# Kernel tuning notes

Hardware: AMD Instinct MI355X
Metric: run time of the kernel (lower is better)

## Reference

```python
import jax, jax.numpy as jnp
import numpy as np

MASK_FILL = -1e10
LOG_2PI = float(np.log(2.0 * np.pi))


def setup_inputs() -> dict:
    key = jax.random.key(0)
    k1, k2, k3 = jax.random.split(key, 3)
    bs, seq_len, emb_dim = 32, 512, 512
    T = 2048
    emb = jax.random.normal(k1, (bs, seq_len, emb_dim), dtype=jnp.float32)
    # positive durations; rescale so the max total duration over the batch == T exactly,
    # matching torch's T = sum(durations).int().max()
    d = jax.random.uniform(k2, (bs, seq_len), dtype=jnp.float32, minval=0.5, maxval=1.0)
    d = d * (T / jnp.max(jnp.sum(d, axis=1)))
    log_sigma = jax.random.normal(k3, (1,), dtype=jnp.float32) * 0.1
    return {"emb": emb, "durations": d, "log_sigma": log_sigma, "T": T}


def reference(emb, durations, log_sigma, T):
    # emb: (bs, S, E); durations: (bs, S); log_sigma: (1,); T: static int
    bs, S, E = emb.shape
    ls = log_sigma[0]
    sigma = jnp.exp(ls)
    # Gaussian centers per token: cumsum - 0.5*dur  -> (bs, S)
    centers = jnp.cumsum(durations, axis=1) - 0.5 * durations
    t = jnp.arange(T, dtype=emb.dtype)  # frame indices (T,)
    # Normal(loc=centers, scale=sigma).log_prob(t + 0.5)  -> (bs, T, S)
    z = (t[None, :, None] + 0.5 - centers[:, None, :]) / sigma
    logp = -0.5 * z * z - ls - 0.5 * LOG_2PI
    # mask out zero-duration tokens
    logp = jnp.where((durations == 0.0)[:, None, :], MASK_FILL, logp)
    w = jax.nn.softmax(logp, axis=2)  # (bs, T, S)
    x = jnp.einsum('bts,bse->bte', w, emb)  # (bs, T, E)
    total = jnp.sum(durations, axis=1)  # (bs,)
    out_mask = t[None, :] < total[:, None]  # (bs, T) bool
    return x, out_mask
```

## Files before the change

### kernel.cpp

```cpp
#include <hip/hip_runtime.h>
#include <math.h>

#define BS 32
#define S_TOK 512
#define E_DIM 512
#define T_FR 2048
#define FPB 32
#define WMAX 36
#define THRESH -25.0f


typedef float vfloat4 __attribute__((ext_vector_type(4)));

struct RowMeta { float m; float inv_l; int lo; int cnt; };

__global__ __launch_bounds__(64) void scan_kernel(
    const float* __restrict__ dur,
    float* __restrict__ centers,
    float* __restrict__ totals) {
  int b = blockIdx.x;
  int lane = threadIdx.x;
  const float* d = dur + b * S_TOK;
  int base = lane * 8;
  double local[8];
  double run = 0.0;
#pragma unroll
  for (int i = 0; i < 8; ++i) { run += (double)d[base + i]; local[i] = run; }
  double sum = run;
#pragma unroll
  for (int off = 1; off < 64; off <<= 1) {
    double v = __shfl_up(sum, off, 64);
    if (lane >= off) sum += v;
  }
  double excl = sum - run;
#pragma unroll
  for (int i = 0; i < 8; ++i) {
    centers[b * S_TOK + base + i] =
        (float)(excl + local[i] - 0.5 * (double)d[base + i]);
  }
  if (lane == 63) totals[b] = (float)sum;
}

__global__ __launch_bounds__(256) void meta_kernel(
    const float* __restrict__ centers,
    const float* __restrict__ log_sigma,
    RowMeta* __restrict__ meta) {
  int b = blockIdx.x >> 3;
  int t = ((blockIdx.x & 7) << 8) + threadIdx.x;

  __shared__ float cbS[S_TOK];
  for (int i = threadIdx.x; i < S_TOK; i += 256)
    cbS[i] = centers[b * S_TOK + i];
  __syncthreads();

  float inv_sigma = expf(-log_sigma[0]);
  float tq = (float)t + 0.5f;

  auto V = [&](int s) {
    float z = (tq - cbS[s]) * inv_sigma;
    return -0.5f * z * z;
  };

  int lo = 0, hi = S_TOK;
  while (lo < hi) {
    int mid = (lo + hi) >> 1;
    if (cbS[mid] < tq) lo = mid + 1; else hi = mid;
  }
  int best; float m;
  if (lo == 0) { best = 0; m = V(0); }
  else if (lo == S_TOK) { best = S_TOK - 1; m = V(best); }
  else {
    float va = V(lo - 1), vb = V(lo);
    if (va >= vb) { best = lo - 1; m = va; } else { best = lo; m = vb; }
  }

  int wl = best, wh = best;
  while (wl > 0 && V(wl - 1) > m + THRESH) --wl;
  while (wh < S_TOK - 1 && V(wh + 1) > m + THRESH) ++wh;

  float l = 0.0f;
  for (int s = wl; s <= wh; ++s) l += expf(V(s) - m);

  RowMeta mt;
  mt.m = m;
  mt.inv_l = 1.0f / l;
  mt.lo = wl;
  mt.cnt = wh - wl + 1;
  meta[b * T_FR + t] = mt;
}

__global__ __launch_bounds__(256) void fused_kernel(
    const float* __restrict__ emb,
    const float* __restrict__ centers,
    const float* __restrict__ log_sigma,
    const RowMeta* __restrict__ meta,
    const float* __restrict__ totals,
    float* __restrict__ x,
    float* __restrict__ mask_out) {
  int id = blockIdx.x;
  int sw = ((id & 7) << 8) + (id >> 3);
  int b = sw >> 6;
  int t0 = (sw & 63) << 5;

  int tid = threadIdx.x;
  int half = tid >> 7;
  int lane = tid & 127;

  __shared__ float wT[WMAX][FPB];
  __shared__ RowMeta metaS[FPB];

  if (tid < FPB) metaS[tid] = meta[b * T_FR + t0 + tid];
  __syncthreads();

  int ulo = metaS[0].lo, uhi = metaS[0].lo + metaS[0].cnt - 1;
#pragma unroll
  for (int f = 1; f < FPB; ++f) {
    ulo = min(ulo, metaS[f].lo);
    uhi = max(uhi, metaS[f].lo + metaS[f].cnt - 1);
  }
  int cnt = min(uhi - ulo + 1, WMAX);

  float inv_sigma = expf(-log_sigma[0]);
  const float* cb = centers + b * S_TOK;

  for (int k = tid; k < cnt * FPB; k += 256) {
    int i = k >> 5, f = k & 31;
    float c = cb[ulo + i];
    float tqf = (float)(t0 + f) + 0.5f;
    float z = (tqf - c) * inv_sigma;
    float v = -0.5f * z * z;
    float e = expf(v - metaS[f].m) * metaS[f].inv_l;
    wT[i][f] = (v - metaS[f].m > THRESH) ? e : 0.0f;
  }
  __syncthreads();

  const vfloat4* e4 =
      (const vfloat4*)emb + ((size_t)(b * S_TOK + ulo)) * (E_DIM / 4) + lane;
  vfloat4 acc[16];
#pragma unroll
  for (int f = 0; f < 16; ++f) acc[f] = (vfloat4){0.f, 0.f, 0.f, 0.f};

  vfloat4 vcur = e4[0];
  vfloat4 vnext = e4[(size_t)min(1, cnt - 1) * (E_DIM / 4)];
  for (int i = 0; i < cnt; ++i) {
    vfloat4 vfut = e4[(size_t)min(i + 2, cnt - 1) * (E_DIM / 4)];
    const vfloat4* wp = (const vfloat4*)&wT[i][half << 4];
    vfloat4 w0 = wp[0], w1 = wp[1], w2 = wp[2], w3 = wp[3];
    acc[0] += w0.x * vcur;  acc[1] += w0.y * vcur;
    acc[2] += w0.z * vcur;  acc[3] += w0.w * vcur;
    acc[4] += w1.x * vcur;  acc[5] += w1.y * vcur;
    acc[6] += w1.z * vcur;  acc[7] += w1.w * vcur;
    acc[8] += w2.x * vcur;  acc[9] += w2.y * vcur;
    acc[10] += w2.z * vcur; acc[11] += w2.w * vcur;
    acc[12] += w3.x * vcur; acc[13] += w3.y * vcur;
    acc[14] += w3.z * vcur; acc[15] += w3.w * vcur;
    vcur = vnext; vnext = vfut;
  }

  vfloat4* xp = (vfloat4*)x +
      ((size_t)(b * T_FR + t0 + (half << 4))) * (E_DIM / 4) + lane;
#pragma unroll
  for (int f = 0; f < 16; ++f)
    xp[(size_t)f * (E_DIM / 4)] = acc[f];

  if (tid < FPB) {
    int t = t0 + tid;
    mask_out[b * T_FR + t] = ((float)t < totals[b]) ? 1.0f : 0.0f;
  }
}

extern "C" void kernel_launch(void* const* d_in, const int* in_sizes, int n_in,
                              void* d_out, int out_size, void* d_ws,
                              size_t ws_size, hipStream_t stream) {
  const float* emb = (const float*)d_in[0];
  const float* dur = (const float*)d_in[1];
  const float* log_sigma = (const float*)d_in[2];

  float* x = (float*)d_out;
  float* mask_out = x + (size_t)BS * T_FR * E_DIM;

  float* centers = (float*)d_ws;
  float* totals = centers + BS * S_TOK;
  RowMeta* meta = (RowMeta*)(totals + 64);

  scan_kernel<<<BS, 64, 0, stream>>>(dur, centers, totals);
  meta_kernel<<<BS * 8, 256, 0, stream>>>(centers, log_sigma, meta);
  fused_kernel<<<(BS * T_FR) / FPB, 256, 0, stream>>>(
      emb, centers, log_sigma, meta, totals, x, mask_out);
}
```

Before: 174.9 us.

## Fuse scan and meta kernels into the main weighted-sum kernel

New measurement: 169.7 us. -3.0%, faster.

```diff
diff --git a/kernel.cpp b/kernel.cpp
--- a/kernel.cpp
+++ b/kernel.cpp
@@ -10,91 +10,15 @@
 #define THRESH -25.0f
 
 
+
 typedef float vfloat4 __attribute__((ext_vector_type(4)));
 
 struct RowMeta { float m; float inv_l; int lo; int cnt; };
 
-__global__ __launch_bounds__(64) void scan_kernel(
+__global__ __launch_bounds__(256) void fused_all(
+    const float* __restrict__ emb,
     const float* __restrict__ dur,
-    float* __restrict__ centers,
-    float* __restrict__ totals) {
-  int b = blockIdx.x;
-  int lane = threadIdx.x;
-  const float* d = dur + b * S_TOK;
-  int base = lane * 8;
-  double local[8];
-  double run = 0.0;
-#pragma unroll
-  for (int i = 0; i < 8; ++i) { run += (double)d[base + i]; local[i] = run; }
-  double sum = run;
-#pragma unroll
-  for (int off = 1; off < 64; off <<= 1) {
-    double v = __shfl_up(sum, off, 64);
-    if (lane >= off) sum += v;
-  }
-  double excl = sum - run;
-#pragma unroll
-  for (int i = 0; i < 8; ++i) {
-    centers[b * S_TOK + base + i] =
-        (float)(excl + local[i] - 0.5 * (double)d[base + i]);
-  }
-  if (lane == 63) totals[b] = (float)sum;
-}
-
-__global__ __launch_bounds__(256) void meta_kernel(
-    const float* __restrict__ centers,
     const float* __restrict__ log_sigma,
-    RowMeta* __restrict__ meta) {
-  int b = blockIdx.x >> 3;
-  int t = ((blockIdx.x & 7) << 8) + threadIdx.x;
-
-  __shared__ float cbS[S_TOK];
-  for (int i = threadIdx.x; i < S_TOK; i += 256)
-    cbS[i] = centers[b * S_TOK + i];
-  __syncthreads();
-
-  float inv_sigma = expf(-log_sigma[0]);
-  float tq = (float)t + 0.5f;
-
-  auto V = [&](int s) {
-    float z = (tq - cbS[s]) * inv_sigma;
-    return -0.5f * z * z;
-  };
-
-  int lo = 0, hi = S_TOK;
-  while (lo < hi) {
-    int mid = (lo + hi) >> 1;
-    if (cbS[mid] < tq) lo = mid + 1; else hi = mid;
-  }
-  int best; float m;
-  if (lo == 0) { best = 0; m = V(0); }
-  else if (lo == S_TOK) { best = S_TOK - 1; m = V(best); }
-  else {
-    float va = V(lo - 1), vb = V(lo);
-    if (va >= vb) { best = lo - 1; m = va; } else { best = lo; m = vb; }
-  }
-
-  int wl = best, wh = best;
-  while (wl > 0 && V(wl - 1) > m + THRESH) --wl;
-  while (wh < S_TOK - 1 && V(wh + 1) > m + THRESH) ++wh;
-
-  float l = 0.0f;
-  for (int s = wl; s <= wh; ++s) l += expf(V(s) - m);
-
-  RowMeta mt;
-  mt.m = m;
-  mt.inv_l = 1.0f / l;
-  mt.lo = wl;
-  mt.cnt = wh - wl + 1;
-  meta[b * T_FR + t] = mt;
-}
-
-__global__ __launch_bounds__(256) void fused_kernel(
-    const float* __restrict__ emb,
-    const float* __restrict__ centers,
-    const float* __restrict__ log_sigma,
-    const RowMeta* __restrict__ meta,
-    const float* __restrict__ totals,
     float* __restrict__ x,
     float* __restrict__ mask_out) {
   int id = blockIdx.x;
@@ -106,10 +30,70 @@
   int half = tid >> 7;
   int lane = tid & 127;
 
+  __shared__ float cbS[S_TOK];
   __shared__ float wT[WMAX][FPB];
   __shared__ RowMeta metaS[FPB];
+  __shared__ double wsumS[4];
+  __shared__ float totalS;
 
-  if (tid < FPB) metaS[tid] = meta[b * T_FR + t0 + tid];
+  {
+    const float* dp = dur + b * S_TOK;
+    int i2 = tid << 1;
+    double d0 = (double)dp[i2];
+    double d1 = (double)dp[i2 + 1];
+    double pair = d0 + d1;
+    double run = pair;
+#pragma unroll
+    for (int off = 1; off < 64; off <<= 1) {
+      double v = __shfl_up(run, off, 64);
+      if ((tid & 63) >= off) run += v;
+    }
+    int w = tid >> 6;
+    if ((tid & 63) == 63) wsumS[w] = run;
+    __syncthreads();
+    double wexcl = 0.0;
+#pragma unroll
+    for (int k = 0; k < 3; ++k) wexcl += (k < w) ? wsumS[k] : 0.0;
+    double incl = wexcl + run;
+    double excl = incl - pair;
+    cbS[i2]     = (float)(excl + d0 - 0.5 * d0);
+    cbS[i2 + 1] = (float)(excl + (d0 + d1) - 0.5 * d1);
+    if (tid == 255) totalS = (float)incl;
+  }
+  __syncthreads();
+
+  float inv_sigma = expf(-log_sigma[0]);
+
+  if (tid < FPB) {
+    float tq = (float)(t0 + tid) + 0.5f;
+    auto V = [&](int s) {
+      float z = (tq - cbS[s]) * inv_sigma;
+      return -0.5f * z * z;
+    };
+    int lo = 0, hi = S_TOK;
+    while (lo < hi) {
+      int mid = (lo + hi) >> 1;
+      if (cbS[mid] < tq) lo = mid + 1; else hi = mid;
+    }
+    int best; float m;
+    if (lo == 0) { best = 0; m = V(0); }
+    else if (lo == S_TOK) { best = S_TOK - 1; m = V(best); }
+    else {
+      float va = V(lo - 1), vb = V(lo);
+      if (va >= vb) { best = lo - 1; m = va; } else { best = lo; m = vb; }
+    }
+    int wl = best, wh = best;
+    while (wl > 0 && V(wl - 1) > m + THRESH) --wl;
+    while (wh < S_TOK - 1 && V(wh + 1) > m + THRESH) ++wh;
+    float l = 0.0f;
+    for (int s = wl; s <= wh; ++s) l += expf(V(s) - m);
+    RowMeta mt;
+    mt.m = m;
+    mt.inv_l = 1.0f / l;
+    mt.lo = wl;
+    mt.cnt = wh - wl + 1;
+    metaS[tid] = mt;
+  }
   __syncthreads();
 
   int ulo = metaS[0].lo, uhi = metaS[0].lo + metaS[0].cnt - 1;
@@ -120,12 +104,9 @@
   }
   int cnt = min(uhi - ulo + 1, WMAX);
 
-  float inv_sigma = expf(-log_sigma[0]);
-  const float* cb = centers + b * S_TOK;
-
   for (int k = tid; k < cnt * FPB; k += 256) {
     int i = k >> 5, f = k & 31;
-    float c = cb[ulo + i];
+    float c = cbS[ulo + i];
     float tqf = (float)(t0 + f) + 0.5f;
     float z = (tqf - c) * inv_sigma;
     float v = -0.5f * z * z;
@@ -165,7 +146,7 @@
 
   if (tid < FPB) {
     int t = t0 + tid;
-    mask_out[b * T_FR + t] = ((float)t < totals[b]) ? 1.0f : 0.0f;
+    mask_out[b * T_FR + t] = ((float)t < totalS) ? 1.0f : 0.0f;
   }
 }
 
@@ -179,12 +160,6 @@
   float* x = (float*)d_out;
   float* mask_out = x + (size_t)BS * T_FR * E_DIM;
 
-  float* centers = (float*)d_ws;
-  float* totals = centers + BS * S_TOK;
-  RowMeta* meta = (RowMeta*)(totals + 64);
-
-  scan_kernel<<<BS, 64, 0, stream>>>(dur, centers, totals);
-  meta_kernel<<<BS * 8, 256, 0, stream>>>(centers, log_sigma, meta);
-  fused_kernel<<<(BS * T_FR) / FPB, 256, 0, stream>>>(
-      emb, centers, log_sigma, meta, totals, x, mask_out);
+  fused_all<<<(BS * T_FR) / FPB, 256, 0, stream>>>(
+      emb, dur, log_sigma, x, mask_out);
 }
```

## Replace shared-memory weight tile with per-wavefront two-frame streaming kernel

Applied to the files above, without the earlier changes.

Result: slower. 180.9 us (+3.4%).

```diff
diff --git a/kernel.cpp b/kernel.cpp
--- a/kernel.cpp
+++ b/kernel.cpp
@@ -5,9 +5,8 @@
 #define S_TOK 512
 #define E_DIM 512
 #define T_FR 2048
-#define FPB 32
-#define WMAX 36
 #define THRESH -25.0f
+
 
 
 typedef float vfloat4 __attribute__((ext_vector_type(4)));
@@ -44,7 +43,9 @@
 __global__ __launch_bounds__(256) void meta_kernel(
     const float* __restrict__ centers,
     const float* __restrict__ log_sigma,
-    RowMeta* __restrict__ meta) {
+    const float* __restrict__ totals,
+    RowMeta* __restrict__ meta,
+    float* __restrict__ mask_out) {
   int b = blockIdx.x >> 3;
   int t = ((blockIdx.x & 7) << 8) + threadIdx.x;
 
@@ -87,86 +88,58 @@
   mt.lo = wl;
   mt.cnt = wh - wl + 1;
   meta[b * T_FR + t] = mt;
+
+  mask_out[b * T_FR + t] = ((float)t < totals[b]) ? 1.0f : 0.0f;
 }
 
-__global__ __launch_bounds__(256) void fused_kernel(
+__global__ __launch_bounds__(256, 8) void stream_kernel(
     const float* __restrict__ emb,
     const float* __restrict__ centers,
     const float* __restrict__ log_sigma,
     const RowMeta* __restrict__ meta,
-    const float* __restrict__ totals,
-    float* __restrict__ x,
-    float* __restrict__ mask_out) {
+    float* __restrict__ x) {
   int id = blockIdx.x;
-  int sw = ((id & 7) << 8) + (id >> 3);
-  int b = sw >> 6;
-  int t0 = (sw & 63) << 5;
+  int sw = ((id & 7) << 10) + (id >> 3);
+  int b = sw >> 8;
+  int t0 = ((sw & 255) << 3) + ((threadIdx.x >> 6) << 1);
+  int lane = threadIdx.x & 63;
 
-  int tid = threadIdx.x;
-  int half = tid >> 7;
-  int lane = tid & 127;
-
-  __shared__ float wT[WMAX][FPB];
-  __shared__ RowMeta metaS[FPB];
-
-  if (tid < FPB) metaS[tid] = meta[b * T_FR + t0 + tid];
-  __syncthreads();
-
-  int ulo = metaS[0].lo, uhi = metaS[0].lo + metaS[0].cnt - 1;
-#pragma unroll
-  for (int f = 1; f < FPB; ++f) {
-    ulo = min(ulo, metaS[f].lo);
-    uhi = max(uhi, metaS[f].lo + metaS[f].cnt - 1);
-  }
-  int cnt = min(uhi - ulo + 1, WMAX);
+  RowMeta m0 = meta[b * T_FR + t0];
+  RowMeta m1 = meta[b * T_FR + t0 + 1];
+  int ulo = min(m0.lo, m1.lo);
+  int uhi = max(m0.lo + m0.cnt, m1.lo + m1.cnt) - 1;
+  int cnt = uhi - ulo + 1;
 
   float inv_sigma = expf(-log_sigma[0]);
-  const float* cb = centers + b * S_TOK;
+  float tq0 = (float)t0 + 0.5f;
+  float tq1 = tq0 + 1.0f;
 
-  for (int k = tid; k < cnt * FPB; k += 256) {
-    int i = k >> 5, f = k & 31;
-    float c = cb[ulo + i];
-    float tqf = (float)(t0 + f) + 0.5f;
-    float z = (tqf - c) * inv_sigma;
-    float v = -0.5f * z * z;
-    float e = expf(v - metaS[f].m) * metaS[f].inv_l;
-    wT[i][f] = (v - metaS[f].m > THRESH) ? e : 0.0f;
-  }
-  __syncthreads();
-
+  const float* cb = centers + b * S_TOK + ulo;
   const vfloat4* e4 =
       (const vfloat4*)emb + ((size_t)(b * S_TOK + ulo)) * (E_DIM / 4) + lane;
-  vfloat4 acc[16];
-#pragma unroll
-  for (int f = 0; f < 16; ++f) acc[f] = (vfloat4){0.f, 0.f, 0.f, 0.f};
 
-  vfloat4 vcur = e4[0];
-  vfloat4 vnext = e4[(size_t)min(1, cnt - 1) * (E_DIM / 4)];
+  vfloat4 a00 = {0.f,0.f,0.f,0.f}, a01 = {0.f,0.f,0.f,0.f};
+  vfloat4 a10 = {0.f,0.f,0.f,0.f}, a11 = {0.f,0.f,0.f,0.f};
+
+  vfloat4 u0 = e4[0], u1 = e4[64];
   for (int i = 0; i < cnt; ++i) {
-    vfloat4 vfut = e4[(size_t)min(i + 2, cnt - 1) * (E_DIM / 4)];
-    const vfloat4* wp = (const vfloat4*)&wT[i][half << 4];
-    vfloat4 w0 = wp[0], w1 = wp[1], w2 = wp[2], w3 = wp[3];
-    acc[0] += w0.x * vcur;  acc[1] += w0.y * vcur;
-    acc[2] += w0.z * vcur;  acc[3] += w0.w * vcur;
-    acc[4] += w1.x * vcur;  acc[5] += w1.y * vcur;
-    acc[6] += w1.z * vcur;  acc[7] += w1.w * vcur;
-    acc[8] += w2.x * vcur;  acc[9] += w2.y * vcur;
-    acc[10] += w2.z * vcur; acc[11] += w2.w * vcur;
-    acc[12] += w3.x * vcur; acc[13] += w3.y * vcur;
-    acc[14] += w3.z * vcur; acc[15] += w3.w * vcur;
-    vcur = vnext; vnext = vfut;
+    int nx = min(i + 1, cnt - 1) * (E_DIM / 4);
+    vfloat4 n0 = e4[nx], n1 = e4[nx + 64];
+    float c = cb[i];
+    float z0 = (tq0 - c) * inv_sigma;
+    float z1 = (tq1 - c) * inv_sigma;
+    float e0 = expf(-0.5f * z0 * z0 - m0.m);
+    float e1 = expf(-0.5f * z1 * z1 - m1.m);
+    a00 += e0 * u0;  a01 += e0 * u1;
+    a10 += e1 * u0;  a11 += e1 * u1;
+    u0 = n0; u1 = n1;
   }
 
-  vfloat4* xp = (vfloat4*)x +
-      ((size_t)(b * T_FR + t0 + (half << 4))) * (E_DIM / 4) + lane;
-#pragma unroll
-  for (int f = 0; f < 16; ++f)
-    xp[(size_t)f * (E_DIM / 4)] = acc[f];
-
-  if (tid < FPB) {
-    int t = t0 + tid;
-    mask_out[b * T_FR + t] = ((float)t < totals[b]) ? 1.0f : 0.0f;
-  }
+  vfloat4* xp = (vfloat4*)x + ((size_t)(b * T_FR + t0)) * (E_DIM / 4) + lane;
+  xp[0]       = a00 * m0.inv_l;
+  xp[64]      = a01 * m0.inv_l;
+  xp[128]     = a10 * m1.inv_l;
+  xp[128+64]  = a11 * m1.inv_l;
 }
 
 extern "C" void kernel_launch(void* const* d_in, const int* in_sizes, int n_in,
@@ -184,7 +157,8 @@
   RowMeta* meta = (RowMeta*)(totals + 64);
 
   scan_kernel<<<BS, 64, 0, stream>>>(dur, centers, totals);
-  meta_kernel<<<BS * 8, 256, 0, stream>>>(centers, log_sigma, meta);
-  fused_kernel<<<(BS * T_FR) / FPB, 256, 0, stream>>>(
-      emb, centers, log_sigma, meta, totals, x, mask_out);
+  meta_kernel<<<BS * 8, 256, 0, stream>>>(centers, log_sigma, totals,
+                                          meta, mask_out);
+  stream_kernel<<<(BS * T_FR) / 8, 256, 0, stream>>>(
+      emb, centers, log_sigma, meta, x);
 }
```
